# Performance work log

Hardware: AMD Instinct MI355X
Metric: run time of the kernel (lower is better)

The kernel has to match this reference:

```python
import jax, jax.numpy as jnp
import numpy as np

N = 100000  # num nodes


def _gcn_conv(x, src, dst, W, b, n_nodes):
    """PyG GCNConv: symmetric normalization with implicit self-loops.
    out = D^{-1/2} (A + I) D^{-1/2} (x W) + b, deg counts in-edges + self-loop.
    """
    h = x @ W  # [N, H]
    ones = jnp.ones(src.shape[0], dtype=x.dtype)
    deg = jax.ops.segment_sum(ones, dst, num_segments=n_nodes) + 1.0  # +1 self-loop
    dinv = jax.lax.rsqrt(deg)  # [N]
    norm = dinv[src] * dinv[dst]  # [E]
    msg = h[src] * norm[:, None]  # gather + scale: memory-bound
    agg = jax.ops.segment_sum(msg, dst, num_segments=n_nodes)
    agg = agg + h * (dinv * dinv)[:, None]  # self-loop contribution
    return agg + b


def setup_inputs() -> dict:
    key = jax.random.key(0)
    k1, k2, k3, k4 = jax.random.split(key, 4)
    F = 64
    E = 1600000
    x = jax.random.normal(k1, (N, F), dtype=jnp.float32)
    edge_index = jax.random.randint(k2, (2, E), 0, N, dtype=jnp.int64)
    W1 = jax.random.normal(k3, (F, F), dtype=jnp.float32) / jnp.sqrt(jnp.float32(F))
    b1 = jnp.zeros((F,), dtype=jnp.float32)
    W2 = jax.random.normal(k4, (F, F), dtype=jnp.float32) / jnp.sqrt(jnp.float32(F))
    b2 = jnp.zeros((F,), dtype=jnp.float32)
    return {"x": x, "edge_index": edge_index, "W1": W1, "b1": b1, "W2": W2, "b2": b2}


def reference(x, edge_index, W1, b1, W2, b2):
    src, dst = edge_index[0], edge_index[1]
    h = _gcn_conv(x, src, dst, W1, b1, N)
    h = jax.nn.relu(h)
    # dropout(p=0.1) is identity in eval mode
    h = _gcn_conv(h, src, dst, W2, b2, N)
    return jax.nn.relu(h)
```

## Files before the change

### kernel.cpp

```cpp
#include <hip/hip_runtime.h>
#include <hip/hip_bf16.h>
#include <stdint.h>

#define NN 100000
#define NE 1600000
#define NBLK 256
#define EPB (NE / NBLK)
#define NBINS 782
#define NCELL (NBINS * NBLK)
#define NSB ((NCELL + 1023) / 1024)
#define GEMMB 782
#define BINCAP 4096


__device__ __forceinline__ unsigned pack_bf16(float a, float b) {
    unsigned ua = __float_as_uint(a);
    unsigned ub = __float_as_uint(b);
    ua += 0x7FFFu + ((ua >> 16) & 1u);
    ub += 0x7FFFu + ((ub >> 16) & 1u);
    return (ua >> 16) | (ub & 0xFFFF0000u);
}
#define BF_LO(u) __uint_as_float((u) << 16)
#define BF_HI(u) __uint_as_float((u) & 0xFFFF0000u)


__device__ __forceinline__ int ei_is64(const int* __restrict__ ei) {
    int z = 0;
#pragma unroll
    for (int i = 0; i < 16; ++i) z |= ei[2 * i + 1];
    return z == 0;
}


__global__ void __launch_bounds__(1024) k_hist(const int* __restrict__ ei,
                                               int* __restrict__ gcount) {
    __shared__ int lbin[NBINS];
    int t = threadIdx.x, blk = blockIdx.x;
    for (int i = t; i < NBINS; i += 1024) lbin[i] = 0;
    __syncthreads();
    int is64 = ei_is64(ei);
    int e0 = blk * EPB;
    if (is64) {
        const int2* p = (const int2*)ei;
        for (int e = e0 + t; e < e0 + EPB; e += 1024)
            atomicAdd(&lbin[p[NE + e].x >> 7], 1);
    } else {
        for (int e = e0 + t; e < e0 + EPB; e += 1024)
            atomicAdd(&lbin[ei[NE + e] >> 7], 1);
    }
    __syncthreads();
    for (int b = t; b < NBINS; b += 1024) gcount[b * NBLK + blk] = lbin[b];
}

__global__ void k_pscan1(const int* __restrict__ g, int* __restrict__ bsum) {
    __shared__ int sh[256];
    int t = threadIdx.x;
    int base = blockIdx.x * 1024 + t * 4;
    int s = 0;
#pragma unroll
    for (int j = 0; j < 4; ++j) { int i = base + j; if (i < NCELL) s += g[i]; }
    sh[t] = s; __syncthreads();
    for (int off = 128; off > 0; off >>= 1) {
        if (t < off) sh[t] += sh[t + off];
        __syncthreads();
    }
    if (t == 0) bsum[blockIdx.x] = sh[0];
}

__global__ void k_pscan23(const int* __restrict__ g, const int* __restrict__ bsum,
                          int* __restrict__ goff) {
    __shared__ int sh[256];
    __shared__ int boffs;
    int t = threadIdx.x;
    int bv = (t < NSB) ? bsum[t] : 0;
    sh[t] = bv; __syncthreads();
    for (int off = 1; off < 256; off <<= 1) {
        int tmp = (t >= off) ? sh[t - off] : 0;
        __syncthreads();
        sh[t] += tmp;
        __syncthreads();
    }
    if (t == blockIdx.x) boffs = sh[t] - bv;
    __syncthreads();
    int base = blockIdx.x * 1024 + t * 4;
    int v[4]; int s = 0;
#pragma unroll
    for (int j = 0; j < 4; ++j) { int i = base + j; v[j] = (i < NCELL) ? g[i] : 0; s += v[j]; }
    __syncthreads();
    sh[t] = s; __syncthreads();
    for (int off = 1; off < 256; off <<= 1) {
        int tmp = (t >= off) ? sh[t - off] : 0;
        __syncthreads();
        sh[t] += tmp;
        __syncthreads();
    }
    int run = sh[t] - s + boffs;
#pragma unroll
    for (int j = 0; j < 4; ++j) {
        int i = base + j;
        if (i < NCELL) { goff[i] = run; run += v[j]; }
    }
}

__global__ void __launch_bounds__(1024) k_scatter(const int* __restrict__ ei,
                                                  const int* __restrict__ goff,
                                                  unsigned* __restrict__ tmp) {
    __shared__ int gpos[NBINS];
    int t = threadIdx.x, blk = blockIdx.x;
    for (int i = t; i < NBINS; i += 1024) gpos[i] = goff[i * NBLK + blk];
    __syncthreads();
    int is64 = ei_is64(ei);
    int e0 = blk * EPB;
    for (int e = e0 + t; e < e0 + EPB; e += 1024) {
        int s, d;
        if (is64) {
            s = ((const int2*)ei)[e].x;
            d = ((const int2*)ei)[NE + e].x;
        } else {
            s = ei[e];
            d = ei[NE + e];
        }
        int b = d >> 7;
        int pos = atomicAdd(&gpos[b], 1);
        tmp[pos] = (unsigned)s | ((unsigned)(d & 127) << 17);
    }
}


__device__ __forceinline__ void gemm_body(int gb, const float* __restrict__ X,
                                          const float* __restrict__ W,
                                          unsigned* __restrict__ Hb) {
    int wid = (gb * 256 + (int)threadIdx.x) >> 6;
    int lane = threadIdx.x & 63;
    int task = __builtin_amdgcn_readfirstlane(wid);
    const int ntasks = ((NN + 63) >> 6) * 2;
    if (task >= ntasks) return;
    int t = task >> 1;
    int ch = task & 1;
    int row = t * 64 + lane;
    int r = row < NN ? row : NN - 1;
    const float4* xp = (const float4*)(X + (size_t)r * 64);
    const float* Wb = W + ch * 32;
    float acc[32];
#pragma unroll
    for (int c = 0; c < 32; ++c) acc[c] = 0.f;
#pragma unroll 4
    for (int k4 = 0; k4 < 16; ++k4) {
        float4 xv = xp[k4];
#pragma unroll
        for (int kj = 0; kj < 4; ++kj) {
            float xk = (kj == 0) ? xv.x : (kj == 1) ? xv.y : (kj == 2) ? xv.z : xv.w;
            const float4* wr = (const float4*)(Wb + (k4 * 4 + kj) * 64);
#pragma unroll
            for (int c4 = 0; c4 < 8; ++c4) {
                float4 wv = wr[c4];
                acc[c4 * 4 + 0] += xk * wv.x;
                acc[c4 * 4 + 1] += xk * wv.y;
                acc[c4 * 4 + 2] += xk * wv.z;
                acc[c4 * 4 + 3] += xk * wv.w;
            }
        }
    }
    uint4* op = (uint4*)(Hb + (size_t)r * 32 + ch * 16);
#pragma unroll
    for (int q = 0; q < 4; ++q) {
        uint4 o;
        o.x = pack_bf16(acc[q * 8 + 0], acc[q * 8 + 1]);
        o.y = pack_bf16(acc[q * 8 + 2], acc[q * 8 + 3]);
        o.z = pack_bf16(acc[q * 8 + 4], acc[q * 8 + 5]);
        o.w = pack_bf16(acc[q * 8 + 6], acc[q * 8 + 7]);
        op[q] = o;
    }
}

__global__ void __launch_bounds__(256) k_gemm(const float* __restrict__ X,
                                              const float* __restrict__ W,
                                              unsigned* __restrict__ Hb) {
    gemm_body(blockIdx.x, X, W, Hb);
}


__global__ void __launch_bounds__(256) k_degcsr_gemm(const unsigned* __restrict__ tmp,
                                                     const int* __restrict__ goff,
                                                     int* __restrict__ rs,
                                                     float* __restrict__ dinv,
                                                     unsigned* __restrict__ csr,
                                                     const float* __restrict__ X,
                                                     const float* __restrict__ W1,
                                                     unsigned* __restrict__ Hb) {
    if (blockIdx.x >= NBINS) {
        gemm_body((int)blockIdx.x - NBINS, X, W1, Hb);
        return;
    }
    __shared__ unsigned cache[BINCAP];
    __shared__ int hist[128];
    __shared__ int cur[128];
    __shared__ int base_sh[128];
    int b = blockIdx.x, t = threadIdx.x;
    if (t < 128) { hist[t] = 0; cur[t] = 0; }
    __syncthreads();
    int bs = goff[b * NBLK];
    int be = (b == NBINS - 1) ? NE : goff[(b + 1) * NBLK];
    for (int e = bs + t; e < be; e += 256) {
        unsigned v = tmp[e];
        int i = e - bs;
        if (i < BINCAP) cache[i] = v;
        atomicAdd(&hist[v >> 17], 1);
    }
    __syncthreads();
    if (t < 128) {
        int node = b * 128 + t;
        if (node < NN) {
            int c = hist[t];
            int loff = 0;
            for (int i = 0; i < t; ++i) loff += hist[i];
            rs[node] = bs + loff;
            base_sh[t] = bs + loff;
            dinv[node] = rsqrtf((float)c + 1.0f);
        } else base_sh[t] = 0;
    }
    if (b == 0 && t == 0) rs[NN] = NE;
    __syncthreads();
    int cnt = be - bs;
    for (int i = t; i < cnt; i += 256) {
        unsigned v = (i < BINCAP) ? cache[i] : tmp[bs + i];
        int dl = v >> 17;
        int lr = atomicAdd(&cur[dl], 1);
        csr[base_sh[dl] + lr] = v & 0x1FFFFu;
    }
}


#define EDGE_ACC(wt, r)                                                       \
    {                                                                         \
        a0 += BF_LO((r).x) * (wt); a1 += BF_HI((r).x) * (wt);                 \
        a2 += BF_LO((r).y) * (wt); a3 += BF_HI((r).y) * (wt);                 \
        a4 += BF_LO((r).z) * (wt); a5 += BF_HI((r).z) * (wt);                 \
        a6 += BF_LO((r).w) * (wt); a7 += BF_HI((r).w) * (wt);                 \
    }

__global__ void __launch_bounds__(256) k_agg(const unsigned* __restrict__ hb,
                                             const int* __restrict__ rs,
                                             const unsigned* __restrict__ csr,
                                             const float* __restrict__ dinv,
                                             const float* __restrict__ bias,
                                             float4* __restrict__ out4) {
    int wid = (blockIdx.x * blockDim.x + threadIdx.x) >> 6;
    int lane = threadIdx.x & 63;
    int node = wid * 2 + (lane >> 5);
    if (node >= NN) return;
    int g = (lane >> 3) & 3;
    int s = lane & 7;
    const char* hbc = (const char*)hb;
    const char* dvc = (const char*)dinv;
    unsigned soff = (unsigned)s << 4;
    float dn = dinv[node];
    int e0 = rs[node], e1 = rs[node + 1];
    float a0 = 0.f, a1 = 0.f, a2 = 0.f, a3 = 0.f;
    float a4 = 0.f, a5 = 0.f, a6 = 0.f, a7 = 0.f;
    int e = e0 + g;
    unsigned p0 = csr[e];
    unsigned p1 = csr[e + 4];
    for (; e + 4 < e1; e += 8) {
        unsigned q0 = csr[e + 8];
        unsigned q1 = csr[e + 12];
        float w0 = *(const float*)(dvc + (size_t)(p0 << 2));
        float w1 = *(const float*)(dvc + (size_t)(p1 << 2));
        uint4 r0 = *(const uint4*)(hbc + (size_t)((p0 << 7) + soff));
        uint4 r1 = *(const uint4*)(hbc + (size_t)((p1 << 7) + soff));
        EDGE_ACC(w0, r0);
        EDGE_ACC(w1, r1);
        p0 = q0; p1 = q1;
    }
    if (e < e1) {
        float w0 = *(const float*)(dvc + (size_t)(p0 << 2));
        uint4 r0 = *(const uint4*)(hbc + (size_t)((p0 << 7) + soff));
        EDGE_ACC(w0, r0);
    }
#pragma unroll
    for (int m = 8; m <= 16; m <<= 1) {
        a0 += __shfl_xor(a0, m); a1 += __shfl_xor(a1, m);
        a2 += __shfl_xor(a2, m); a3 += __shfl_xor(a3, m);
        a4 += __shfl_xor(a4, m); a5 += __shfl_xor(a5, m);
        a6 += __shfl_xor(a6, m); a7 += __shfl_xor(a7, m);
    }
    if ((lane & 31) < 8) {
        uint4 r = *(const uint4*)(hbc + (size_t)(((unsigned)node << 7) + soff));
        const float4* bp = (const float4*)(bias + s * 8);
        float4 b0 = bp[0], b1v = bp[1];
        float4 o0, o1;
        o0.x = fmaxf((a0 + BF_LO(r.x) * dn) * dn + b0.x, 0.f);
        o0.y = fmaxf((a1 + BF_HI(r.x) * dn) * dn + b0.y, 0.f);
        o0.z = fmaxf((a2 + BF_LO(r.y) * dn) * dn + b0.z, 0.f);
        o0.w = fmaxf((a3 + BF_HI(r.y) * dn) * dn + b0.w, 0.f);
        o1.x = fmaxf((a4 + BF_LO(r.z) * dn) * dn + b1v.x, 0.f);
        o1.y = fmaxf((a5 + BF_HI(r.z) * dn) * dn + b1v.y, 0.f);
        o1.z = fmaxf((a6 + BF_LO(r.w) * dn) * dn + b1v.z, 0.f);
        o1.w = fmaxf((a7 + BF_HI(r.w) * dn) * dn + b1v.w, 0.f);
        out4[(size_t)node * 16 + s * 2] = o0;
        out4[(size_t)node * 16 + s * 2 + 1] = o1;
    }
}


extern "C" void kernel_launch(void* const* d_in, const int* in_sizes, int n_in,
                              void* d_out, int out_size, void* d_ws, size_t ws_size,
                              hipStream_t stream) {
    const float* x  = (const float*)d_in[0];
    const int* ei   = (const int*)d_in[1];
    const float* W1 = (const float*)d_in[2];
    const float* b1 = (const float*)d_in[3];
    const float* W2 = (const float*)d_in[4];
    const float* b2 = (const float*)d_in[5];

    char* ws = (char*)d_ws;
    size_t off = 0;
    auto alloc = [&](size_t bytes) -> char* {
        char* p = ws + off;
        off = (off + bytes + 511) & ~(size_t)511;
        return p;
    };
    int*      gcount= (int*)alloc((size_t)NCELL * 4);
    int*      goff  = (int*)alloc((size_t)NCELL * 4);
    int*      bsum  = (int*)alloc((size_t)NSB * 4);
    unsigned* tmp   = (unsigned*)alloc((size_t)NE * 4);
    unsigned* csr   = (unsigned*)alloc((size_t)NE * 4);
    int*      rs    = (int*)alloc((size_t)(NN + 1) * 4);
    float*    dinv  = (float*)alloc((size_t)NN * 4);
    unsigned* hbuf  = (unsigned*)alloc((size_t)NN * 32 * 4);
    float*    hmid  = (float*)d_out;

    k_hist<<<NBLK, 1024, 0, stream>>>(ei, gcount);
    k_pscan1<<<NSB, 256, 0, stream>>>(gcount, bsum);
    k_pscan23<<<NSB, 256, 0, stream>>>(gcount, bsum, goff);
    k_scatter<<<NBLK, 1024, 0, stream>>>(ei, goff, tmp);
    k_degcsr_gemm<<<NBINS + GEMMB, 256, 0, stream>>>(tmp, goff, rs, dinv, csr,
                                                     x, W1, hbuf);
    k_agg<<<(NN / 2) * 64 / 256, 256, 0, stream>>>(hbuf, rs, csr, dinv, b1,
                                                   (float4*)hmid);
    k_gemm<<<GEMMB, 256, 0, stream>>>(hmid, W2, hbuf);
    k_agg<<<(NN / 2) * 64 / 256, 256, 0, stream>>>(hbuf, rs, csr, dinv, b2,
                                                   (float4*)d_out);
}
```

Before: 231.3 us.

## Remap GEMM so each lane owns an output column with W held in registers

Rewrites the dense X·W GEMM mapping. Previously each lane computed one row and 32 output columns, reading W rows via float4 loads. Now each lane keeps one column of W in 64 registers, and a wave processes 16 rows, four at a time, with X rows broadcast across the wave. Adjacent lanes are combined by shuffle to pack bf16 pairs, and the grid size is doubled to match. This aims to cut redundant W loads and make X reads coalesced broadcasts, at the cost of half the lanes idling during stores and narrower 4-byte writes.

```diff
diff --git a/kernel.cpp b/kernel.cpp
--- a/kernel.cpp
+++ b/kernel.cpp
@@ -9,7 +9,7 @@
 #define NBINS 782
 #define NCELL (NBINS * NBLK)
 #define NSB ((NCELL + 1023) / 1024)
-#define GEMMB 782
+#define GEMMB 1563
 #define BINCAP 4096
 
 
@@ -130,46 +130,45 @@
 __device__ __forceinline__ void gemm_body(int gb, const float* __restrict__ X,
                                           const float* __restrict__ W,
                                           unsigned* __restrict__ Hb) {
-    int wid = (gb * 256 + (int)threadIdx.x) >> 6;
     int lane = threadIdx.x & 63;
-    int task = __builtin_amdgcn_readfirstlane(wid);
-    const int ntasks = ((NN + 63) >> 6) * 2;
-    if (task >= ntasks) return;
-    int t = task >> 1;
-    int ch = task & 1;
-    int row = t * 64 + lane;
-    int r = row < NN ? row : NN - 1;
-    const float4* xp = (const float4*)(X + (size_t)r * 64);
-    const float* Wb = W + ch * 32;
-    float acc[32];
-#pragma unroll
-    for (int c = 0; c < 32; ++c) acc[c] = 0.f;
-#pragma unroll 4
-    for (int k4 = 0; k4 < 16; ++k4) {
-        float4 xv = xp[k4];
-#pragma unroll
-        for (int kj = 0; kj < 4; ++kj) {
-            float xk = (kj == 0) ? xv.x : (kj == 1) ? xv.y : (kj == 2) ? xv.z : xv.w;
-            const float4* wr = (const float4*)(Wb + (k4 * 4 + kj) * 64);
-#pragma unroll
-            for (int c4 = 0; c4 < 8; ++c4) {
-                float4 wv = wr[c4];
-                acc[c4 * 4 + 0] += xk * wv.x;
-                acc[c4 * 4 + 1] += xk * wv.y;
-                acc[c4 * 4 + 2] += xk * wv.z;
-                acc[c4 * 4 + 3] += xk * wv.w;
-            }
+    int wave = __builtin_amdgcn_readfirstlane(gb * 4 + ((int)threadIdx.x >> 6));
+    const int nwaves = (NN + 15) / 16;
+    if (wave >= nwaves) return;
+    float wcol[64];
+#pragma unroll
+    for (int k = 0; k < 64; ++k) wcol[k] = W[k * 64 + lane];
+    for (int rg = 0; rg < 4; ++rg) {
+        int rbase = wave * 16 + rg * 4;
+        int r0 = rbase     < NN ? rbase     : NN - 1;
+        int r1 = rbase + 1 < NN ? rbase + 1 : NN - 1;
+        int r2 = rbase + 2 < NN ? rbase + 2 : NN - 1;
+        int r3 = rbase + 3 < NN ? rbase + 3 : NN - 1;
+        const float4* x0 = (const float4*)(X + (size_t)r0 * 64);
+        const float4* x1 = (const float4*)(X + (size_t)r1 * 64);
+        const float4* x2 = (const float4*)(X + (size_t)r2 * 64);
+        const float4* x3 = (const float4*)(X + (size_t)r3 * 64);
+        float a0 = 0.f, a1 = 0.f, a2 = 0.f, a3 = 0.f;
+#pragma unroll
+        for (int k4 = 0; k4 < 16; ++k4) {
+            float4 v0 = x0[k4], v1 = x1[k4], v2 = x2[k4], v3 = x3[k4];
+            a0 += v0.x * wcol[k4 * 4 + 0]; a1 += v1.x * wcol[k4 * 4 + 0];
+            a2 += v2.x * wcol[k4 * 4 + 0]; a3 += v3.x * wcol[k4 * 4 + 0];
+            a0 += v0.y * wcol[k4 * 4 + 1]; a1 += v1.y * wcol[k4 * 4 + 1];
+            a2 += v2.y * wcol[k4 * 4 + 1]; a3 += v3.y * wcol[k4 * 4 + 1];
+            a0 += v0.z * wcol[k4 * 4 + 2]; a1 += v1.z * wcol[k4 * 4 + 2];
+            a2 += v2.z * wcol[k4 * 4 + 2]; a3 += v3.z * wcol[k4 * 4 + 2];
+            a0 += v0.w * wcol[k4 * 4 + 3]; a1 += v1.w * wcol[k4 * 4 + 3];
+            a2 += v2.w * wcol[k4 * 4 + 3]; a3 += v3.w * wcol[k4 * 4 + 3];
         }
-    }
-    uint4* op = (uint4*)(Hb + (size_t)r * 32 + ch * 16);
-#pragma unroll
-    for (int q = 0; q < 4; ++q) {
-        uint4 o;
-        o.x = pack_bf16(acc[q * 8 + 0], acc[q * 8 + 1]);
-        o.y = pack_bf16(acc[q * 8 + 2], acc[q * 8 + 3]);
-        o.z = pack_bf16(acc[q * 8 + 4], acc[q * 8 + 5]);
-        o.w = pack_bf16(acc[q * 8 + 6], acc[q * 8 + 7]);
-        op[q] = o;
+        float p0 = __shfl_xor(a0, 1), p1 = __shfl_xor(a1, 1);
+        float p2 = __shfl_xor(a2, 1), p3 = __shfl_xor(a3, 1);
+        if (!(lane & 1)) {
+            int w = lane >> 1;
+            Hb[(size_t)r0 * 32 + w] = pack_bf16(a0, p0);
+            Hb[(size_t)r1 * 32 + w] = pack_bf16(a1, p1);
+            Hb[(size_t)r2 * 32 + w] = pack_bf16(a2, p2);
+            Hb[(size_t)r3 * 32 + w] = pack_bf16(a3, p3);
+        }
     }
 }
 
```

Result: slower. 235.9 us (+2.0%).

## Stage X rows in padded LDS and split GEMM output into four 16-column waves

Applied to the files above, without the earlier changes.

The GEMM body now has each 256-thread block cooperatively load 64 rows of X into a padded shared-memory tile with coalesced float4 reads. Each of the four waves then computes 16 output columns for those rows, instead of two waves per 64 rows computing 32 columns from strided per-lane global loads. The GEMM block count doubles and the shared buffer is aliased between the GEMM and degree/CSR roles. The aim is better coalescing, fewer accumulator registers and higher occupancy. The cost is LDS traffic and a barrier, and the GEMM blocks now carry the full shared allocation.

```diff
diff --git a/kernel.cpp b/kernel.cpp
--- a/kernel.cpp
+++ b/kernel.cpp
@@ -9,8 +9,9 @@
 #define NBINS 782
 #define NCELL (NBINS * NBLK)
 #define NSB ((NCELL + 1023) / 1024)
-#define GEMMB 782
+#define GEMMB 1563
 #define BINCAP 4096
+#define SMEM_BYTES (BINCAP * 4 + 3 * 128 * 4)
 
 
 __device__ __forceinline__ unsigned pack_bf16(float a, float b) {
@@ -129,41 +130,52 @@
 
 __device__ __forceinline__ void gemm_body(int gb, const float* __restrict__ X,
                                           const float* __restrict__ W,
-                                          unsigned* __restrict__ Hb) {
-    int wid = (gb * 256 + (int)threadIdx.x) >> 6;
-    int lane = threadIdx.x & 63;
-    int task = __builtin_amdgcn_readfirstlane(wid);
-    const int ntasks = ((NN + 63) >> 6) * 2;
-    if (task >= ntasks) return;
-    int t = task >> 1;
-    int ch = task & 1;
-    int row = t * 64 + lane;
-    int r = row < NN ? row : NN - 1;
-    const float4* xp = (const float4*)(X + (size_t)r * 64);
-    const float* Wb = W + ch * 32;
-    float acc[32];
-#pragma unroll
-    for (int c = 0; c < 32; ++c) acc[c] = 0.f;
+                                          unsigned* __restrict__ Hb,
+                                          float* xt) {
+    int t = threadIdx.x;
+    int lane = t & 63;
+    int wv = t >> 6;
+    int rbase = gb * 64;
+    const float4* xg = (const float4*)X;
+#pragma unroll
+    for (int j = 0; j < 4; ++j) {
+        int idx = j * 256 + t;
+        int row = idx >> 4;
+        int q = idx & 15;
+        int gr = rbase + row;
+        int r = gr < NN ? gr : NN - 1;
+        float4 v = xg[(size_t)r * 16 + q];
+        float* dst = xt + row * 65 + q * 4;
+        dst[0] = v.x; dst[1] = v.y; dst[2] = v.z; dst[3] = v.w;
+    }
+    __syncthreads();
+    int grow = rbase + lane;
+    int r = grow < NN ? grow : NN - 1;
+    int ch = __builtin_amdgcn_readfirstlane(wv);
+    const float* Wb = W + ch * 16;
+    const float* xr = xt + lane * 65;
+    float acc[16];
+#pragma unroll
+    for (int c = 0; c < 16; ++c) acc[c] = 0.f;
 #pragma unroll 4
     for (int k4 = 0; k4 < 16; ++k4) {
-        float4 xv = xp[k4];
 #pragma unroll
         for (int kj = 0; kj < 4; ++kj) {
-            float xk = (kj == 0) ? xv.x : (kj == 1) ? xv.y : (kj == 2) ? xv.z : xv.w;
+            float xk = xr[k4 * 4 + kj];
             const float4* wr = (const float4*)(Wb + (k4 * 4 + kj) * 64);
 #pragma unroll
-            for (int c4 = 0; c4 < 8; ++c4) {
-                float4 wv = wr[c4];
-                acc[c4 * 4 + 0] += xk * wv.x;
-                acc[c4 * 4 + 1] += xk * wv.y;
-                acc[c4 * 4 + 2] += xk * wv.z;
-                acc[c4 * 4 + 3] += xk * wv.w;
+            for (int c4 = 0; c4 < 4; ++c4) {
+                float4 wv4 = wr[c4];
+                acc[c4 * 4 + 0] += xk * wv4.x;
+                acc[c4 * 4 + 1] += xk * wv4.y;
+                acc[c4 * 4 + 2] += xk * wv4.z;
+                acc[c4 * 4 + 3] += xk * wv4.w;
             }
         }
     }
-    uint4* op = (uint4*)(Hb + (size_t)r * 32 + ch * 16);
-#pragma unroll
-    for (int q = 0; q < 4; ++q) {
+    uint4* op = (uint4*)(Hb + (size_t)r * 32 + ch * 8);
+#pragma unroll
+    for (int q = 0; q < 2; ++q) {
         uint4 o;
         o.x = pack_bf16(acc[q * 8 + 0], acc[q * 8 + 1]);
         o.y = pack_bf16(acc[q * 8 + 2], acc[q * 8 + 3]);
@@ -176,7 +188,8 @@
 __global__ void __launch_bounds__(256) k_gemm(const float* __restrict__ X,
                                               const float* __restrict__ W,
                                               unsigned* __restrict__ Hb) {
-    gemm_body(blockIdx.x, X, W, Hb);
+    __shared__ __align__(16) char smem[SMEM_BYTES];
+    gemm_body(blockIdx.x, X, W, Hb, (float*)smem);
 }
 
 
@@ -188,14 +201,15 @@
                                                      const float* __restrict__ X,
                                                      const float* __restrict__ W1,
                                                      unsigned* __restrict__ Hb) {
+    __shared__ __align__(16) char smem[SMEM_BYTES];
     if (blockIdx.x >= NBINS) {
-        gemm_body((int)blockIdx.x - NBINS, X, W1, Hb);
+        gemm_body((int)blockIdx.x - NBINS, X, W1, Hb, (float*)smem);
         return;
     }
-    __shared__ unsigned cache[BINCAP];
-    __shared__ int hist[128];
-    __shared__ int cur[128];
-    __shared__ int base_sh[128];
+    unsigned* cache  = (unsigned*)smem;
+    int*      hist   = (int*)(smem + BINCAP * 4);
+    int*      cur    = hist + 128;
+    int*      base_sh= cur + 128;
     int b = blockIdx.x, t = threadIdx.x;
     if (t < 128) { hist[t] = 0; cur[t] = 0; }
     __syncthreads();
```

Measured after the change: 226.6 us. 2.0% less time.
